# Performance work log

Hardware: AMD Instinct MI355X
Metric: run time of the kernel (lower is better)

Reference implementation:

```python
import jax, jax.numpy as jnp
import numpy as np

THRESHOLD = 0.5     # overlap_thresh
NEG_POS = 3         # negative:positive ratio
VAR = (0.1, 0.2)    # cfg['variance']


def point_form(pr):
    # cxcywh -> xmin,ymin,xmax,ymax
    return jnp.concatenate([pr[:, :2] - pr[:, 2:] / 2, pr[:, :2] + pr[:, 2:] / 2], axis=1)


def jaccard(a, b):
    # a: [N,4] point-form truths, b: [P,4] point-form priors -> IoU [N,P]
    lt = jnp.maximum(a[:, None, :2], b[None, :, :2])
    rb = jnp.minimum(a[:, None, 2:], b[None, :, 2:])
    wh = jnp.clip(rb - lt, 0.0)
    inter = wh[..., 0] * wh[..., 1]
    area_a = ((a[:, 2] - a[:, 0]) * (a[:, 3] - a[:, 1]))[:, None]
    area_b = ((b[:, 2] - b[:, 0]) * (b[:, 3] - b[:, 1]))[None, :]
    return inter / (area_a + area_b - inter)


def encode(matched, priors):
    # matched: [P,4] point-form, priors: [P,4] cxcywh
    g_cxcy = ((matched[:, :2] + matched[:, 2:]) / 2 - priors[:, :2]) / (VAR[0] * priors[:, 2:])
    g_wh = jnp.log((matched[:, 2:] - matched[:, :2]) / priors[:, 2:]) / VAR[1]
    return jnp.concatenate([g_cxcy, g_wh], axis=1)


def match_one(truths, labels, priors):
    # truths [N,4], labels [N], priors [P,4] cxcywh
    N = truths.shape[0]
    P = priors.shape[0]
    overlaps = jaccard(truths, point_form(priors))          # [N,P]
    best_prior_idx = jnp.argmax(overlaps, axis=1)           # [N] best prior per truth
    best_truth_overlap = jnp.max(overlaps, axis=0)          # [P]
    best_truth_idx = jnp.argmax(overlaps, axis=0)           # [P]
    # ensure each truth's best prior is kept (overlap forced to 2)
    best_truth_overlap = best_truth_overlap.at[best_prior_idx].set(2.0)
    hit = best_prior_idx[:, None] == jnp.arange(P)[None, :]  # [N,P]
    chosen = jnp.max(jnp.where(hit, jnp.arange(N)[:, None], -1), axis=0)
    best_truth_idx = jnp.where(chosen >= 0, chosen, best_truth_idx)
    matched = truths[best_truth_idx]                        # [P,4]
    conf = labels[best_truth_idx].astype(jnp.int32) + 1
    conf = jnp.where(best_truth_overlap < THRESHOLD, 0, conf)
    return encode(matched, priors), conf


def smooth_l1(x):
    ax = jnp.abs(x)
    return jnp.where(ax < 1.0, 0.5 * ax * ax, ax - 0.5)


def multibox_loss(loc_data, conf_data, priors, targets):
    num, P, C = conf_data.shape
    truths = targets[..., :4]
    labels = targets[..., 4]
    loc_t, conf_t = jax.vmap(match_one, in_axes=(0, 0, None))(truths, labels, priors)
    pos = conf_t > 0                                        # [B,P]

    # localization loss over positives
    loss_l = jnp.sum(jnp.where(pos[..., None], smooth_l1(loc_data - loc_t), 0.0))

    # hard-negative mining score: logsumexp - conf[label clamped to {0,1}]
    batch_conf = jax.lax.stop_gradient(conf_data).reshape(-1, C)
    conf_flat = conf_t.reshape(-1)
    clamped = jnp.where(conf_flat != 0, 1, conf_flat)
    # replicate torch nonzero()-indexing quirk: row 0 also set to 1 if any positive exists
    clamped = clamped.at[0].set(jnp.where(jnp.any(conf_flat != 0), 1, clamped[0]))
    lse = jax.scipy.special.logsumexp(batch_conf, axis=1)
    loss_c = lse - jnp.take_along_axis(batch_conf, clamped[:, None], axis=1)[:, 0]
    loss_c = loss_c.reshape(num, P)
    loss_c = jnp.where(pos, 0.0, loss_c)
    # rank of each prior by descending mining loss
    idx_rank = jnp.argsort(jnp.argsort(-loss_c, axis=1), axis=1)
    num_pos = jnp.sum(pos.astype(jnp.int32), axis=1, keepdims=True)  # [B,1]
    num_neg = jnp.clip(NEG_POS * num_pos, None, P - 1)
    neg = idx_rank < num_neg
    sel = pos | neg

    # confidence cross-entropy over selected priors, original labels as targets
    logp = jax.nn.log_softmax(conf_data, axis=-1)           # [B,P,C]
    ce = -jnp.take_along_axis(logp, conf_t[..., None], axis=-1)[..., 0]
    loss_conf = jnp.sum(jnp.where(sel, ce, 0.0))

    Nf = jnp.sum(num_pos).astype(jnp.float32)
    return loss_l / Nf, loss_conf / Nf


def setup_inputs() -> dict:
    key = jax.random.key(0)
    k1, k2, k3, k4, k5, k6, k7 = jax.random.split(key, 7)
    B, P, C, NOBJ = 128, 8732, 21, 20
    loc_data = jax.random.normal(k1, (B, P, 4), jnp.float32)
    conf_data = jax.random.normal(k2, (B, P, C), jnp.float32)
    pcxy = jax.random.uniform(k3, (P, 2), jnp.float32, 0.05, 0.95)
    pwh = jax.random.uniform(k4, (P, 2), jnp.float32, 0.05, 0.4)
    priors = jnp.concatenate([pcxy, pwh], axis=1)           # cxcywh
    mins = jax.random.uniform(k5, (B, NOBJ, 2), jnp.float32, 0.0, 0.6)
    wh = jax.random.uniform(k6, (B, NOBJ, 2), jnp.float32, 0.05, 0.35)
    lab = jax.random.randint(k7, (B, NOBJ), 0, C - 1).astype(jnp.float32)
    targets = jnp.concatenate([mins, mins + wh, lab[..., None]], axis=-1)
    return {"loc_data": loc_data, "conf_data": conf_data, "priors": priors, "targets": targets}


def reference(loc_data, conf_data, priors, targets):
    return multibox_loss(loc_data, conf_data, priors, targets)
```

## Files before the change

kernel.cpp:

```cpp
#include <hip/hip_runtime.h>

#define PP 8732
#define NB 20
#define NC 21
#define BTH 256
#define NCH 35
#define BTS 1024
#define NWS (BTS/64)

__device__ __forceinline__ float sl1(float d){
  float a = fabsf(d);
  return a < 1.0f ? 0.5f*a*a : a - 0.5f;
}

__device__ __forceinline__ float wave_max64(float x){
  int t;
  t = __builtin_amdgcn_update_dpp(0, __float_as_int(x), 0x111, 0xF, 0xF, true); x = fmaxf(x, __int_as_float(t));
  t = __builtin_amdgcn_update_dpp(0, __float_as_int(x), 0x112, 0xF, 0xF, true); x = fmaxf(x, __int_as_float(t));
  t = __builtin_amdgcn_update_dpp(0, __float_as_int(x), 0x114, 0xF, 0xF, true); x = fmaxf(x, __int_as_float(t));
  t = __builtin_amdgcn_update_dpp(0, __float_as_int(x), 0x118, 0xF, 0xF, true); x = fmaxf(x, __int_as_float(t));
  t = __builtin_amdgcn_update_dpp(0, __float_as_int(x), 0x142, 0xF, 0xF, true); x = fmaxf(x, __int_as_float(t));
  t = __builtin_amdgcn_update_dpp(0, __float_as_int(x), 0x143, 0xF, 0xF, true); x = fmaxf(x, __int_as_float(t));
  return __int_as_float(__builtin_amdgcn_readlane(__float_as_int(x), 63));
}

extern "C" __global__ void __launch_bounds__(BTH)
mb_main(const float* __restrict__ conf_data,
        const float* __restrict__ priors,
        const float* __restrict__ targets,
        float* __restrict__ rankneg,
        unsigned char* __restrict__ meta,
        unsigned long long* __restrict__ keys2)
{
  const int b = blockIdx.x, chunk = blockIdx.y;
  const int tid = threadIdx.x, lane = tid & 63, wid = tid >> 6;
  const int q0 = chunk*BTH + wid*64;
  const int cnt = (q0 < PP) ? ((PP - q0 < 64) ? (PP - q0) : 64) : 0;

  __shared__ float s_buf[4][64*NC];
  __shared__ float4 s_tr4[NB];
  __shared__ unsigned long long s_keys[4][NB];

  if (tid < NB*4){
    int n = tid>>2, k2 = tid&3;
    ((float*)s_tr4)[tid] = targets[((long)b*NB + n)*5 + k2];
  }
  if (lane < NB) s_keys[wid][lane] = 0ULL;
  __syncthreads();

  if (cnt == 64){
    const float4* cb4 = reinterpret_cast<const float4*>(conf_data + ((long)b*PP + q0)*NC);
    float4* sb4 = reinterpret_cast<float4*>(s_buf[wid]);
    #pragma unroll
    for (int ii=0; ii<6; ii++){
      int i = ii*64 + lane;
      if (i < 336) sb4[i] = cb4[i];
    }
  } else if (cnt > 0){
    const float4* cb4 = reinterpret_cast<const float4*>(conf_data + ((long)b*PP + q0)*NC);
    float4* sb4 = reinterpret_cast<float4*>(s_buf[wid]);
    const int tot4 = (cnt*NC) >> 2;
    for (int i=lane; i<tot4; i+=64) sb4[i] = cb4[i];
  }

  const bool valid = (lane < cnt);
  const int p  = q0 + lane;
  const int pl = valid ? p : 0;

  const float* v = s_buf[wid] + lane*NC;
  float m = v[0];
  #pragma unroll
  for (int c=1;c<NC;c++) m = fmaxf(m, v[c]);
  float s = 0.f;
  #pragma unroll
  for (int c=0;c<NC;c++) s += __expf(v[c]-m);
  float lse = __logf(s) + m;
  if (valid) rankneg[(long)b*PP + p] = lse - v[0];

  float4 pr = reinterpret_cast<const float4*>(priors)[pl];
  float bx1 = pr.x - pr.z*0.5f, by1 = pr.y - pr.w*0.5f;
  float bx2 = pr.x + pr.z*0.5f, by2 = pr.y + pr.w*0.5f;
  float area_b = (bx2-bx1)*(by2-by1);
  float bestov = -1.0f; int bestn = 0;

  for (int n=0;n<NB;n++){
    float4 t = s_tr4[n];
    float lx=fmaxf(t.x,bx1), ly=fmaxf(t.y,by1);
    float rx=fminf(t.z,bx2), ry=fminf(t.w,by2);
    float iw=fmaxf(rx-lx,0.f), ih=fmaxf(ry-ly,0.f);
    float inter = iw*ih;
    float aa = (t.z-t.x)*(t.w-t.y);
    float iou = inter * __builtin_amdgcn_rcpf(aa + area_b - inter);
    if (iou > bestov){ bestov=iou; bestn=n; }

    float iouv = valid ? iou : -1.0f;
    float wmax = wave_max64(iouv);
    unsigned long long mk = __ballot(valid && (iou == wmax));
    if (mk){
      int wlane = __ffsll((long long)mk) - 1;
      if (lane == wlane)
        s_keys[wid][n] = ((unsigned long long)__float_as_uint(iou)<<32)
                       | (unsigned long long)(0xFFFFFFFFu - (unsigned)p);
    }
  }

  if (valid) meta[(long)b*PP + p] = (unsigned char)((bestn<<1) | (bestov >= 0.5f ? 1 : 0));

  __syncthreads();
  if (tid < NB){
    unsigned long long mx = s_keys[0][tid];
    #pragma unroll
    for (int w=1;w<4;w++) if (s_keys[w][tid] > mx) mx = s_keys[w][tid];
    keys2[((long)b*NCH + chunk)*NB + tid] = mx;
  }
}

extern "C" __global__ void __launch_bounds__(BTS)
mb_select(const float* __restrict__ loc_data,
          const float* __restrict__ conf_data,
          const float* __restrict__ priors,
          const float* __restrict__ targets,
          const float* __restrict__ rankneg,
          const unsigned char* __restrict__ meta,
          const unsigned long long* __restrict__ keys2,
          float* __restrict__ rowres, int* __restrict__ ticket,
          float* __restrict__ out, int Bn)
{
  const int b = blockIdx.x, tid = threadIdx.x, lane = tid & 63, wid = tid >> 6;
  __shared__ float s_val[PP];
  __shared__ unsigned int s_meta4[PP/4];
  __shared__ float4 s_tr4[NB];
  __shared__ float s_lab[NB];
  __shared__ int   s_bp[NB];
  __shared__ int   s_cnt[2][NWS];
  __shared__ float s_fa[NWS], s_fb[NWS], s_fc[NWS];
  __shared__ int   s_ia[NWS];
  __shared__ float s_rowll, s_rowpc, s_delta;
  __shared__ int   s_npos, s_spec, s_last;
  unsigned char* s_meta = (unsigned char*)s_meta4;
  float4* sv4 = reinterpret_cast<float4*>(s_val);

  const float4* rr = reinterpret_cast<const float4*>(rankneg + (long)b*PP);
  for (int i=tid;i<PP/4;i+=BTS) sv4[i]=rr[i];
  const unsigned int* mr = reinterpret_cast<const unsigned int*>(meta + (long)b*PP);
  for (int i=tid;i<PP/4;i+=BTS) s_meta4[i]=mr[i];
  if (tid < NB*5){
    int n = tid/5, k2 = tid-n*5;
    float vv = targets[((long)b*NB+n)*5+k2];
    if (k2<4) ((float*)&s_tr4[n])[k2]=vv; else s_lab[n]=vv;
  }
  if (tid < NB){
    unsigned long long mx = 0ULL;
    #pragma unroll
    for (int c=0;c<NCH;c++){
      unsigned long long kk = keys2[((long)b*NCH + c)*NB + tid];
      if (kk > mx) mx = kk;
    }
    s_bp[tid] = (int)(0xFFFFFFFFu - (unsigned)(mx & 0xFFFFFFFFULL));
  }
  if (tid==0){ s_spec=0; s_delta=0.f; }
  __syncthreads();

  if (tid==0){
    for (int n=0;n<NB;n++) s_meta[s_bp[n]] = (unsigned char)((n<<1)|1);
  }
  __syncthreads();

  float ll=0.f, pc=0.f; int np=0;
  for (int p=tid;p<PP;p+=BTS){
    int mt = s_meta[p];
    if (mt & 1){
      np++;
      int n = mt>>1;
      int ct = (int)s_lab[n] + 1;
      const float* cp = conf_data + ((long)b*PP+p)*NC;
      float v0 = cp[0], vct = cp[ct];
      pc += s_val[p] + v0 - vct;
      float4 t = s_tr4[n];
      float4 pr = reinterpret_cast<const float4*>(priors)[p];
      float4 ld = reinterpret_cast<const float4*>(loc_data)[(long)b*PP+p];
      float g0 = ((t.x+t.z)*0.5f - pr.x)/(0.1f*pr.z);
      float g1 = ((t.y+t.w)*0.5f - pr.y)/(0.1f*pr.w);
      float g2 = __logf((t.z-t.x)/pr.z)/0.2f;
      float g3 = __logf((t.w-t.y)/pr.w)/0.2f;
      ll += sl1(ld.x-g0)+sl1(ld.y-g1)+sl1(ld.z-g2)+sl1(ld.w-g3);
      s_val[p] = 0.f;
    } else if (b==0 && p==0){
      float v0 = conf_data[0], v1 = conf_data[1];
      float r0 = s_val[0];
      float r0p = r0 + v0 - v1;
      s_delta = r0 - r0p;
      s_spec = 1;
      s_val[0] = r0p;
    }
  }
  #pragma unroll
  for (int o=32;o;o>>=1){
    ll += __shfl_down(ll,o,64);
    pc += __shfl_down(pc,o,64);
    np += __shfl_down(np,o,64);
  }
  if (lane==0){ s_fa[wid]=ll; s_fb[wid]=pc; s_ia[wid]=np; }
  __syncthreads();

  float4 rv0 = sv4[tid];
  float4 rv1 = sv4[tid+1024];
  float4 rv2 = (tid < PP/4-2048) ? sv4[tid+2048]
                                 : make_float4(0.f,0.f,0.f,0.f);

  if (tid==0){
    float a=0.f,c2=0.f; int ni=0;
    for (int w=0;w<NWS;w++){ a+=s_fa[w]; c2+=s_fb[w]; ni+=s_ia[w]; }
    s_rowll=a; s_rowpc=c2; s_npos=ni;
  }
  __syncthreads();
  const int num_pos = s_npos;
  int k = num_pos*3; if (k > PP-1) k = PP-1;

  float negsum = 0.f;
  if (k > 0){
    unsigned lo=0u, hi=0x7f800000u;
    int it=0;
    while (lo < hi){
      unsigned mid = lo + ((hi - lo + 1u) >> 1);
      int c = (__float_as_uint(rv0.x)>=mid) + (__float_as_uint(rv0.y)>=mid)
            + (__float_as_uint(rv0.z)>=mid) + (__float_as_uint(rv0.w)>=mid)
            + (__float_as_uint(rv1.x)>=mid) + (__float_as_uint(rv1.y)>=mid)
            + (__float_as_uint(rv1.z)>=mid) + (__float_as_uint(rv1.w)>=mid)
            + (__float_as_uint(rv2.x)>=mid) + (__float_as_uint(rv2.y)>=mid)
            + (__float_as_uint(rv2.z)>=mid) + (__float_as_uint(rv2.w)>=mid);
      #pragma unroll
      for (int o=32;o;o>>=1) c += __shfl_down(c,o,64);
      int sl2 = it&1;
      if (lane==0) s_cnt[sl2][wid]=c;
      __syncthreads();
      int tot=0;
      #pragma unroll
      for (int w=0;w<NWS;w++) tot += s_cnt[sl2][w];
      if (tot >= k) lo = mid; else hi = mid - 1u;
      it++;
    }
    const unsigned vstar = lo;

    int cg=0; float sg=0.f;
    #define ACC(x) if (__float_as_uint(x)>vstar){cg++;sg+=(x);}
    ACC(rv0.x) ACC(rv0.y) ACC(rv0.z) ACC(rv0.w)
    ACC(rv1.x) ACC(rv1.y) ACC(rv1.z) ACC(rv1.w)
    ACC(rv2.x) ACC(rv2.y) ACC(rv2.z) ACC(rv2.w)
    #undef ACC
    #pragma unroll
    for (int o=32;o;o>>=1){ cg += __shfl_down(cg,o,64); sg += __shfl_down(sg,o,64); }
    __syncthreads();
    if (lane==0){ s_ia[wid]=cg; s_fa[wid]=sg; }
    __syncthreads();
    if (tid==0){
      int cG=0; float sumG=0.f;
      for (int w=0;w<NWS;w++){ cG+=s_ia[w]; sumG+=s_fa[w]; }
      int tie = k - cG;
      negsum = sumG + (float)tie * __uint_as_float(vstar);
      if (b==0 && s_spec && __float_as_uint(s_val[0]) >= vstar) negsum += s_delta;
    }
  }

  if (tid==0){
    rowres[b*4+0] = s_rowll;
    rowres[b*4+1] = s_rowpc + negsum;
    rowres[b*4+2] = (float)num_pos;
    __threadfence();
    int t = atomicAdd(ticket, 1);
    s_last = (t == gridDim.x - 1) ? 1 : 0;
  }
  __syncthreads();

  if (s_last){
    __threadfence();
    float a0=0.f, a1=0.f, a2=0.f;
    for (int i=tid;i<Bn;i+=BTS){
      a0 += rowres[i*4+0]; a1 += rowres[i*4+1]; a2 += rowres[i*4+2];
    }
    #pragma unroll
    for (int o=32;o;o>>=1){
      a0 += __shfl_down(a0,o,64);
      a1 += __shfl_down(a1,o,64);
      a2 += __shfl_down(a2,o,64);
    }
    if (lane==0){ s_fa[wid]=a0; s_fb[wid]=a1; s_fc[wid]=a2; }
    __syncthreads();
    if (tid==0){
      float A0=0.f,A1=0.f,A2=0.f;
      for (int w=0;w<NWS;w++){ A0+=s_fa[w]; A1+=s_fb[w]; A2+=s_fc[w]; }
      out[0] = A0/A2;
      out[1] = A1/A2;
    }
  }
}

extern "C" void kernel_launch(void* const* d_in, const int* in_sizes, int n_in,
                              void* d_out, int out_size, void* d_ws, size_t ws_size,
                              hipStream_t stream) {
  const float* loc     = (const float*)d_in[0];
  const float* conf    = (const float*)d_in[1];
  const float* priors  = (const float*)d_in[2];
  const float* targets = (const float*)d_in[3];
  float* out = (float*)d_out;
  int B = in_sizes[0] / (PP*4);

  char* ws = (char*)d_ws;
  int*   ticket = (int*)ws;
  float* rowres = (float*)(ws + 64);
  unsigned long long* keys2 = (unsigned long long*)(ws + 4096);
  size_t off_rank = 4096 + (size_t)B*NCH*NB*8;
  float* rankneg = (float*)(ws + off_rank);
  unsigned char* metaa = (unsigned char*)(ws + off_rank + (size_t)B*PP*4);

  hipMemsetAsync(d_ws, 0, 64, stream);
  hipLaunchKernelGGL(mb_main,   dim3(B, NCH), dim3(BTH), 0, stream,
                     conf, priors, targets, rankneg, metaa, keys2);
  hipLaunchKernelGGL(mb_select, dim3(B), dim3(BTS), 0, stream,
                     loc, conf, priors, targets, rankneg, metaa, keys2,
                     rowres, ticket, out, B);
}
```

Before: 211.8 us.

## Overlap conf loads with IoU loop via LDS-direct loads; streamline select reductions

After: 202.1 us. 1.05x faster.

```diff
diff --git a/kernel.cpp b/kernel.cpp
--- a/kernel.cpp
+++ b/kernel.cpp
@@ -22,6 +22,16 @@
   t = __builtin_amdgcn_update_dpp(0, __float_as_int(x), 0x142, 0xF, 0xF, true); x = fmaxf(x, __int_as_float(t));
   t = __builtin_amdgcn_update_dpp(0, __float_as_int(x), 0x143, 0xF, 0xF, true); x = fmaxf(x, __int_as_float(t));
   return __int_as_float(__builtin_amdgcn_readlane(__float_as_int(x), 63));
+}
+
+__device__ __forceinline__ int wave_sum64_lane63(int x){
+  x += __builtin_amdgcn_update_dpp(0, x, 0x111, 0xF, 0xF, true);
+  x += __builtin_amdgcn_update_dpp(0, x, 0x112, 0xF, 0xF, true);
+  x += __builtin_amdgcn_update_dpp(0, x, 0x114, 0xF, 0xF, true);
+  x += __builtin_amdgcn_update_dpp(0, x, 0x118, 0xF, 0xF, true);
+  x += __builtin_amdgcn_update_dpp(0, x, 0x142, 0xF, 0xF, true);
+  x += __builtin_amdgcn_update_dpp(0, x, 0x143, 0xF, 0xF, true);
+  return x;
 }
 
 extern "C" __global__ void __launch_bounds__(BTH)
@@ -37,25 +47,32 @@
   const int q0 = chunk*BTH + wid*64;
   const int cnt = (q0 < PP) ? ((PP - q0 < 64) ? (PP - q0) : 64) : 0;
 
-  __shared__ float s_buf[4][64*NC];
-  __shared__ float4 s_tr4[NB];
+  __shared__ __align__(16) float s_buf[4][64*NC];
   __shared__ unsigned long long s_keys[4][NB];
 
-  if (tid < NB*4){
-    int n = tid>>2, k2 = tid&3;
-    ((float*)s_tr4)[tid] = targets[((long)b*NB + n)*5 + k2];
-  }
-  if (lane < NB) s_keys[wid][lane] = 0ULL;
-  __syncthreads();
+  const bool valid = (lane < cnt);
+  const int p  = q0 + lane;
+  const int pl = valid ? p : 0;
+
+  float tx=0.f, ty=0.f, tz=0.f, tw=0.f;
+  if (lane < NB){
+    const float* tp = targets + ((long)b*NB + lane)*5;
+    tx = tp[0]; ty = tp[1]; tz = tp[2]; tw = tp[3];
+  }
+  float4 pr = reinterpret_cast<const float4*>(priors)[pl];
 
   if (cnt == 64){
-    const float4* cb4 = reinterpret_cast<const float4*>(conf_data + ((long)b*PP + q0)*NC);
-    float4* sb4 = reinterpret_cast<float4*>(s_buf[wid]);
-    #pragma unroll
-    for (int ii=0; ii<6; ii++){
-      int i = ii*64 + lane;
-      if (i < 336) sb4[i] = cb4[i];
-    }
+    const char* g = (const char*)(conf_data + ((long)b*PP + q0)*NC) + lane*16;
+    char* l0 = (char*)&s_buf[wid][0];
+    #pragma unroll
+    for (int i=0;i<5;i++)
+      __builtin_amdgcn_global_load_lds(
+        (const __attribute__((address_space(1))) void*)(g + i*1024),
+        (__attribute__((address_space(3))) void*)(l0 + i*1024), 16, 0, 0);
+    if (lane < 16)
+      __builtin_amdgcn_global_load_lds(
+        (const __attribute__((address_space(1))) void*)(g + 5*1024),
+        (__attribute__((address_space(3))) void*)(l0 + 5*1024), 16, 0, 0);
   } else if (cnt > 0){
     const float4* cb4 = reinterpret_cast<const float4*>(conf_data + ((long)b*PP + q0)*NC);
     float4* sb4 = reinterpret_cast<float4*>(s_buf[wid]);
@@ -63,48 +80,58 @@
     for (int i=lane; i<tot4; i+=64) sb4[i] = cb4[i];
   }
 
-  const bool valid = (lane < cnt);
-  const int p  = q0 + lane;
-  const int pl = valid ? p : 0;
-
-  const float* v = s_buf[wid] + lane*NC;
-  float m = v[0];
-  #pragma unroll
-  for (int c=1;c<NC;c++) m = fmaxf(m, v[c]);
-  float s = 0.f;
-  #pragma unroll
-  for (int c=0;c<NC;c++) s += __expf(v[c]-m);
-  float lse = __logf(s) + m;
-  if (valid) rankneg[(long)b*PP + p] = lse - v[0];
-
-  float4 pr = reinterpret_cast<const float4*>(priors)[pl];
   float bx1 = pr.x - pr.z*0.5f, by1 = pr.y - pr.w*0.5f;
   float bx2 = pr.x + pr.z*0.5f, by2 = pr.y + pr.w*0.5f;
   float area_b = (bx2-bx1)*(by2-by1);
+  float area_a = (tz-tx)*(tw-ty);
   float bestov = -1.0f; int bestn = 0;
-
-  for (int n=0;n<NB;n++){
-    float4 t = s_tr4[n];
-    float lx=fmaxf(t.x,bx1), ly=fmaxf(t.y,by1);
-    float rx=fminf(t.z,bx2), ry=fminf(t.w,by2);
-    float iw=fmaxf(rx-lx,0.f), ih=fmaxf(ry-ly,0.f);
-    float inter = iw*ih;
-    float aa = (t.z-t.x)*(t.w-t.y);
-    float iou = inter * __builtin_amdgcn_rcpf(aa + area_b - inter);
-    if (iou > bestov){ bestov=iou; bestn=n; }
-
-    float iouv = valid ? iou : -1.0f;
-    float wmax = wave_max64(iouv);
-    unsigned long long mk = __ballot(valid && (iou == wmax));
-    if (mk){
+  unsigned long long mykey = 0ULL;
+
+  if (cnt > 0){
+    #pragma unroll 4
+    for (int n=0;n<NB;n++){
+      float t_x = __int_as_float(__builtin_amdgcn_readlane(__float_as_int(tx), n));
+      float t_y = __int_as_float(__builtin_amdgcn_readlane(__float_as_int(ty), n));
+      float t_z = __int_as_float(__builtin_amdgcn_readlane(__float_as_int(tz), n));
+      float t_w = __int_as_float(__builtin_amdgcn_readlane(__float_as_int(tw), n));
+      float aa  = __int_as_float(__builtin_amdgcn_readlane(__float_as_int(area_a), n));
+      float lx=fmaxf(t_x,bx1), ly=fmaxf(t_y,by1);
+      float rx=fminf(t_z,bx2), ry=fminf(t_w,by2);
+      float iw=fmaxf(rx-lx,0.f), ih=fmaxf(ry-ly,0.f);
+      float inter = iw*ih;
+      float iou = inter * __builtin_amdgcn_rcpf(aa + area_b - inter);
+      if (iou > bestov){ bestov=iou; bestn=n; }
+
+      float iouv = valid ? iou : -1.0f;
+      float wmax = wave_max64(iouv);
+      unsigned long long mk = __ballot(valid && (iou == wmax));
       int wlane = __ffsll((long long)mk) - 1;
-      if (lane == wlane)
-        s_keys[wid][n] = ((unsigned long long)__float_as_uint(iou)<<32)
-                       | (unsigned long long)(0xFFFFFFFFu - (unsigned)p);
-    }
-  }
-
-  if (valid) meta[(long)b*PP + p] = (unsigned char)((bestn<<1) | (bestov >= 0.5f ? 1 : 0));
+      unsigned long long key = ((unsigned long long)__float_as_uint(wmax)<<32)
+                             | (unsigned long long)(0xFFFFFFFFu - (unsigned)(q0 + wlane));
+      if (lane == n) mykey = key;
+    }
+  }
+  if (lane < NB) s_keys[wid][lane] = mykey;
+
+  if (cnt > 0){
+    asm volatile("s_waitcnt vmcnt(0)" ::: "memory");
+
+    const float* v = s_buf[wid] + lane*NC;
+    float vv[NC];
+    #pragma unroll
+    for (int c=0;c<NC;c++) vv[c] = v[c];
+    float m = vv[0];
+    #pragma unroll
+    for (int c=1;c<NC;c++) m = fmaxf(m, vv[c]);
+    float s = 0.f;
+    #pragma unroll
+    for (int c=0;c<NC;c++) s += __expf(vv[c]-m);
+    float lse = __logf(s) + m;
+    if (valid){
+      rankneg[(long)b*PP + p] = lse - vv[0];
+      meta[(long)b*PP + p] = (unsigned char)((bestn<<1) | (bestov >= 0.5f ? 1 : 0));
+    }
+  }
 
   __syncthreads();
   if (tid < NB){
@@ -127,16 +154,16 @@
           float* __restrict__ out, int Bn)
 {
   const int b = blockIdx.x, tid = threadIdx.x, lane = tid & 63, wid = tid >> 6;
-  __shared__ float s_val[PP];
-  __shared__ unsigned int s_meta4[PP/4];
+  __shared__ __align__(16) float s_val[PP];
+  __shared__ __align__(16) unsigned int s_meta4[PP/4];
   __shared__ float4 s_tr4[NB];
   __shared__ float s_lab[NB];
   __shared__ int   s_bp[NB];
-  __shared__ int   s_cnt[2][NWS];
+  __shared__ int   s_tot[32];
   __shared__ float s_fa[NWS], s_fb[NWS], s_fc[NWS];
   __shared__ int   s_ia[NWS];
-  __shared__ float s_rowll, s_rowpc, s_delta;
-  __shared__ int   s_npos, s_spec, s_last;
+  __shared__ float s_rowll, s_rowpc;
+  __shared__ int   s_npos, s_last;
   unsigned char* s_meta = (unsigned char*)s_meta4;
   float4* sv4 = reinterpret_cast<float4*>(s_val);
 
@@ -158,13 +185,43 @@
     }
     s_bp[tid] = (int)(0xFFFFFFFFu - (unsigned)(mx & 0xFFFFFFFFULL));
   }
-  if (tid==0){ s_spec=0; s_delta=0.f; }
+  if (tid < 32) s_tot[tid] = 0;
   __syncthreads();
 
   if (tid==0){
     for (int n=0;n<NB;n++) s_meta[s_bp[n]] = (unsigned char)((n<<1)|1);
   }
   __syncthreads();
+
+  float4 rv0 = sv4[tid];
+  float4 rv1 = sv4[tid+1024];
+  float4 rv2 = (tid < PP/4-2048) ? sv4[tid+2048]
+                                 : make_float4(0.f,0.f,0.f,0.f);
+  unsigned mm0 = s_meta4[tid];
+  unsigned mm1 = s_meta4[tid+1024];
+  unsigned mm2 = (tid < PP/4-2048) ? s_meta4[tid+2048] : 0u;
+  if (mm0 & 0x00000001u) rv0.x = 0.f;
+  if (mm0 & 0x00000100u) rv0.y = 0.f;
+  if (mm0 & 0x00010000u) rv0.z = 0.f;
+  if (mm0 & 0x01000000u) rv0.w = 0.f;
+  if (mm1 & 0x00000001u) rv1.x = 0.f;
+  if (mm1 & 0x00000100u) rv1.y = 0.f;
+  if (mm1 & 0x00010000u) rv1.z = 0.f;
+  if (mm1 & 0x01000000u) rv1.w = 0.f;
+  if (mm2 & 0x00000001u) rv2.x = 0.f;
+  if (mm2 & 0x00000100u) rv2.y = 0.f;
+  if (mm2 & 0x00010000u) rv2.z = 0.f;
+  if (mm2 & 0x01000000u) rv2.w = 0.f;
+
+  int spec = 0; float delta = 0.f, val0 = 0.f;
+  if (b==0 && tid==0 && !(mm0 & 1u)){
+    float v0 = conf_data[0], v1 = conf_data[1];
+    float r0 = rv0.x;
+    float r0p = r0 + v0 - v1;
+    delta = r0 - r0p;
+    spec = 1;
+    rv0.x = r0p; val0 = r0p;
+  }
 
   float ll=0.f, pc=0.f; int np=0;
   for (int p=tid;p<PP;p+=BTS){
@@ -177,21 +234,13 @@
       float v0 = cp[0], vct = cp[ct];
       pc += s_val[p] + v0 - vct;
       float4 t = s_tr4[n];
-      float4 pr = reinterpret_cast<const float4*>(priors)[p];
+      float4 prr = reinterpret_cast<const float4*>(priors)[p];
       float4 ld = reinterpret_cast<const float4*>(loc_data)[(long)b*PP+p];
-      float g0 = ((t.x+t.z)*0.5f - pr.x)/(0.1f*pr.z);
-      float g1 = ((t.y+t.w)*0.5f - pr.y)/(0.1f*pr.w);
-      float g2 = __logf((t.z-t.x)/pr.z)/0.2f;
-      float g3 = __logf((t.w-t.y)/pr.w)/0.2f;
+      float g0 = ((t.x+t.z)*0.5f - prr.x)/(0.1f*prr.z);
+      float g1 = ((t.y+t.w)*0.5f - prr.y)/(0.1f*prr.w);
+      float g2 = __logf((t.z-t.x)/prr.z)/0.2f;
+      float g3 = __logf((t.w-t.y)/prr.w)/0.2f;
       ll += sl1(ld.x-g0)+sl1(ld.y-g1)+sl1(ld.z-g2)+sl1(ld.w-g3);
-      s_val[p] = 0.f;
-    } else if (b==0 && p==0){
-      float v0 = conf_data[0], v1 = conf_data[1];
-      float r0 = s_val[0];
-      float r0p = r0 + v0 - v1;
-      s_delta = r0 - r0p;
-      s_spec = 1;
-      s_val[0] = r0p;
     }
   }
   #pragma unroll
@@ -202,12 +251,6 @@
   }
   if (lane==0){ s_fa[wid]=ll; s_fb[wid]=pc; s_ia[wid]=np; }
   __syncthreads();
-
-  float4 rv0 = sv4[tid];
-  float4 rv1 = sv4[tid+1024];
-  float4 rv2 = (tid < PP/4-2048) ? sv4[tid+2048]
-                                 : make_float4(0.f,0.f,0.f,0.f);
-
   if (tid==0){
     float a=0.f,c2=0.f; int ni=0;
     for (int w=0;w<NWS;w++){ a+=s_fa[w]; c2+=s_fb[w]; ni+=s_ia[w]; }
@@ -229,14 +272,10 @@
             + (__float_as_uint(rv1.z)>=mid) + (__float_as_uint(rv1.w)>=mid)
             + (__float_as_uint(rv2.x)>=mid) + (__float_as_uint(rv2.y)>=mid)
             + (__float_as_uint(rv2.z)>=mid) + (__float_as_uint(rv2.w)>=mid);
-      #pragma unroll
-      for (int o=32;o;o>>=1) c += __shfl_down(c,o,64);
-      int sl2 = it&1;
-      if (lane==0) s_cnt[sl2][wid]=c;
+      c = wave_sum64_lane63(c);
+      if (lane==63) atomicAdd(&s_tot[it], c);
       __syncthreads();
-      int tot=0;
-      #pragma unroll
-      for (int w=0;w<NWS;w++) tot += s_cnt[sl2][w];
+      int tot = s_tot[it];
       if (tot >= k) lo = mid; else hi = mid - 1u;
       it++;
     }
@@ -258,7 +297,7 @@
       for (int w=0;w<NWS;w++){ cG+=s_ia[w]; sumG+=s_fa[w]; }
       int tie = k - cG;
       negsum = sumG + (float)tie * __uint_as_float(vstar);
-      if (b==0 && s_spec && __float_as_uint(s_val[0]) >= vstar) negsum += s_delta;
+      if (b==0 && spec && __float_as_uint(val0) >= vstar) negsum += delta;
     }
   }
 
```
